# Kernel optimization log

Measured on AMD Instinct MI355X. Metric: run time of the kernel, lower is better.

## Reference

```python
import jax, jax.numpy as jnp
import numpy as np

KS = 5          # B-spline kernel_size per pseudo-coordinate dim
DIM = 2         # pseudo-coordinate dimensionality
NUM_GRAPHS = 64


def spline_conv(x, src, dst, edge_attr, W, root, bias):
    """Degree-1 open B-spline conv (torch-spline-conv semantics, aggr='mean').
    x: [N,Cin], edge_attr: [E,DIM] in [0,1], W: [KS**DIM,Cin,Cout]."""
    N = x.shape[0]
    E = src.shape[0]
    v = edge_attr * (KS - 1)                                   # [E,DIM]
    k_lo = jnp.clip(jnp.floor(v), 0, KS - 2).astype(jnp.int32) # lower knot index
    frac = v - k_lo.astype(v.dtype)                            # [E,DIM]
    # Precompute x @ W_k for all K kernel weights per node: [N,K,Cout]
    xW = jnp.einsum('nc,kco->nko', x, W)
    msg = jnp.zeros((E, W.shape[2]), x.dtype)
    # 2^DIM = 4 nonzero basis products for degree-1 splines
    for bits in ((0, 0), (0, 1), (1, 0), (1, 1)):
        b = jnp.ones((E,), x.dtype)
        wi = jnp.zeros((E,), jnp.int32)
        stride = 1
        for d, bit in enumerate(bits):
            b = b * (frac[:, d] if bit else (1.0 - frac[:, d]))
            wi = wi + (k_lo[:, d] + bit) * stride
            stride *= KS
        msg = msg + b[:, None] * xW[src, wi]                   # gather [E,Cout]
    agg = jax.ops.segment_sum(msg, dst, num_segments=N)
    deg = jax.ops.segment_sum(jnp.ones((E,), x.dtype), dst, num_segments=N)
    agg = agg / jnp.maximum(deg, 1.0)[:, None]                 # mean aggregation
    return agg + x @ root + bias


def setup_inputs() -> dict:
    key = jax.random.key(0)
    ks = jax.random.split(key, 12)
    N, E = 20000, 320000
    Cin, H, O = 1, 32, 10
    K = KS * KS
    p = lambda k, s: jax.random.normal(k, s, jnp.float32) * 0.1
    return {
        'x': jax.random.normal(ks[0], (N, Cin), jnp.float32),
        'edge_attr': jax.random.uniform(ks[1], (E, DIM), jnp.float32),
        'W1': p(ks[2], (K, Cin, H)), 'root1': p(ks[3], (Cin, H)), 'b1': jnp.zeros((H,), jnp.float32),
        'W2': p(ks[4], (K, H, 2 * H)), 'root2': p(ks[5], (H, 2 * H)), 'b2': jnp.zeros((2 * H,), jnp.float32),
        'Wf1': p(ks[6], (2 * H, 128)), 'bf1': jnp.zeros((128,), jnp.float32),
        'Wf2': p(ks[7], (128, O)), 'bf2': jnp.zeros((O,), jnp.float32),
        'edge_index': jax.random.randint(ks[8], (2, E), 0, N),
        'batch': jnp.sort(jax.random.randint(ks[9], (N,), 0, NUM_GRAPHS)),
    }


def reference(x, edge_attr, W1, root1, b1, W2, root2, b2, Wf1, bf1, Wf2, bf2, edge_index, batch):
    src, dst = edge_index[0], edge_index[1]
    h = jax.nn.relu(spline_conv(x, src, dst, edge_attr, W1, root1, b1))
    h = jax.nn.relu(spline_conv(h, src, dst, edge_attr, W2, root2, b2))
    # global mean pool over graphs
    gsum = jax.ops.segment_sum(h, batch, num_segments=NUM_GRAPHS)
    cnt = jax.ops.segment_sum(jnp.ones((h.shape[0],), h.dtype), batch, num_segments=NUM_GRAPHS)
    g = gsum / jnp.maximum(cnt, 1.0)[:, None]
    g = jax.nn.relu(g @ Wf1 + bf1)
    return jax.nn.log_softmax(g @ Wf2 + bf2, axis=1)
```

## Files before the change

kernel.cpp:

```cpp
#include <hip/hip_runtime.h>
#include <hip/hip_fp16.h>
#include <math.h>

#define KK 25
#define H1C 32
#define H2C 64
#define FCC 128
#define NCLS 10
#define NG 64
#define M1 32
#define M2 16
#define NHB 128
#define HBIN 10240

typedef _Float16 v8h __attribute__((ext_vector_type(8)));
typedef float v4f __attribute__((ext_vector_type(4)));

__global__ __launch_bounds__(256) void hist_kernel(
    const int* __restrict__ edge_index, int E, int N,
    int* __restrict__ part) {
    __shared__ int hs[HBIN];
    int b = blockIdx.x, tid = threadIdx.x;
    int per = (E + NHB - 1) / NHB;
    int beg = b * per, end = min(E, beg + per);
    for (int lo = 0; lo < N; lo += HBIN) {
        int sz = min(HBIN, N - lo);
        __syncthreads();
        for (int i = tid; i < sz; i += 256) hs[i] = 0;
        __syncthreads();
        for (int i = beg + tid; i < end; i += 256) {
            int d = edge_index[E + i] - lo;
            if ((unsigned)d < (unsigned)sz) atomicAdd(&hs[d], 1);
        }
        __syncthreads();
        for (int i = tid; i < sz; i += 256) part[(size_t)b * N + lo + i] = hs[i];
    }
}

__global__ void merge_kernel(const int* __restrict__ part, int N,
                             int* __restrict__ degi) {
    int n = blockIdx.x * 256 + threadIdx.x;
    if (n >= N) return;
    int s = 0;
    for (int b = 0; b < NHB; b++) s += part[(size_t)b * N + n];
    degi[n] = s;
}

__global__ void scan1_kernel(const int* __restrict__ degi, int N,
                             int* __restrict__ incl, int* __restrict__ bsum) {
    __shared__ int s[256];
    int tid = threadIdx.x;
    int i = blockIdx.x * 256 + tid;
    int v = (i < N) ? degi[i] : 0;
    s[tid] = v;
    __syncthreads();
    for (int off = 1; off < 256; off <<= 1) {
        int t = (tid >= off) ? s[tid - off] : 0;
        __syncthreads();
        s[tid] += t;
        __syncthreads();
    }
    if (i < N) incl[i] = s[tid];
    if (tid == 255) bsum[blockIdx.x] = s[255];
}

__global__ void scan2_kernel(int* __restrict__ bsum, int nb) {
    __shared__ int s[256];
    int tid = threadIdx.x;
    int v = (tid < nb) ? bsum[tid] : 0;
    s[tid] = v;
    __syncthreads();
    for (int off = 1; off < 256; off <<= 1) {
        int t = (tid >= off) ? s[tid - off] : 0;
        __syncthreads();
        s[tid] += t;
        __syncthreads();
    }
    if (tid < nb) bsum[tid] = s[tid] - v;
}

__global__ void scan3_kernel(const int* __restrict__ incl, const int* __restrict__ degi,
                             const int* __restrict__ bsum, int N,
                             int* __restrict__ rowst, int* __restrict__ cur) {
    int i = blockIdx.x * 256 + threadIdx.x;
    if (i >= N) return;
    int r = incl[i] - degi[i] + bsum[blockIdx.x];
    rowst[i] = r;
    cur[i] = r;
}

__global__ void bucket_kernel(const float* __restrict__ edge_attr,
                              const int* __restrict__ edge_index, int E,
                              int* __restrict__ cur, int4* __restrict__ es) {
    int e = blockIdx.x * blockDim.x + threadIdx.x;
    if (e >= E) return;
    float v0 = edge_attr[2 * e + 0] * 4.0f;
    float v1 = edge_attr[2 * e + 1] * 4.0f;
    int k0 = (int)floorf(v0); k0 = min(max(k0, 0), 3);
    int k1 = (int)floorf(v1); k1 = min(max(k1, 0), 3);
    float f0 = v0 - (float)k0, f1 = v1 - (float)k1;
    int dst = edge_index[E + e];
    int pos = atomicAdd(&cur[dst], 1);
    es[pos] = make_int4(edge_index[e], (dst << 8) | (k0 + 5 * k1),
                        __float_as_int(f0), __float_as_int(f1));
}

__global__ void w2t_kernel(const float* __restrict__ W2, __half* __restrict__ W2t) {
    int idx = blockIdx.x * 256 + threadIdx.x;
    if (idx >= KK * H2C * H1C) return;
    int c = idx & 31, o = (idx >> 5) & 63, k = idx >> 11;
    W2t[idx] = __float2half(W2[(k * H1C + c) * H2C + o]);
}

__global__ __launch_bounds__(256) void l1_kernel(
    const float* __restrict__ x,
    const int* __restrict__ rowst, const int* __restrict__ degi,
    const int4* __restrict__ es,
    const float* __restrict__ W1, const float* __restrict__ root1,
    const float* __restrict__ b1, int N, int E,
    float* __restrict__ h1, __half* __restrict__ h1f) {
    __shared__ float w1s[KK * H1C];
    __shared__ float agg1[M1 * H1C];
    __shared__ int4 eb[8][32];
    __shared__ float xb[8][32];
    int tid = threadIdx.x;
    for (int i = tid; i < KK * H1C; i += 256) w1s[i] = W1[i];
    for (int i = tid; i < M1 * H1C; i += 256) agg1[i] = 0.0f;
    __syncthreads();
    int g = tid >> 5, o = tid & 31;
    int n0 = blockIdx.x * M1;
    int blkBeg = rowst[n0];
    int blkEnd = (n0 + M1 < N) ? rowst[n0 + M1] : E;
    int total = blkEnd - blkBeg;
    int per = (total + 7) >> 3;
    int wBeg = blkBeg + g * per;
    int wEnd = min(blkEnd, wBeg + per);
    int curDst = -1;
    float acc = 0.0f;
    for (int base = wBeg; base < wEnd; base += 32) {
        int m = min(32, wEnd - base);
        if (o < m) {
            int4 ed = es[base + o];
            eb[g][o] = ed;
            xb[g][o] = x[ed.x];
        }
        for (int j = 0; j < m; j++) {
            int4 ed = eb[g][j];
            float xs = xb[g][j];
            int dst = ed.y >> 8;
            if (dst != curDst) {
                if (curDst >= 0) atomicAdd(&agg1[(curDst - n0) * H1C + o], acc);
                acc = 0.0f;
                curDst = dst;
            }
            float f0 = __int_as_float(ed.z), f1 = __int_as_float(ed.w);
            float g0 = 1.0f - f0, g1 = 1.0f - f1;
            int kb = (ed.y & 0xff) << 5;
            float coef = g0 * g1 * w1s[kb + o] + f0 * g1 * w1s[kb + 32 + o] +
                         g0 * f1 * w1s[kb + 160 + o] + f0 * f1 * w1s[kb + 192 + o];
            acc = fmaf(xs, coef, acc);
        }
    }
    if (curDst >= 0) atomicAdd(&agg1[(curDst - n0) * H1C + o], acc);
    __syncthreads();
#pragma unroll
    for (int i = 0; i < 4; i++) {
        int ln = g + 8 * i;
        int n = n0 + ln;
        if (n < N) {
            float rdeg = 1.0f / fmaxf((float)degi[n], 1.0f);
            float hv = fmaxf(agg1[ln * H1C + o] * rdeg + x[n] * root1[o] + b1[o], 0.0f);
            h1[n * H1C + o] = hv;
            h1f[n * H1C + o] = __float2half(hv);
        }
    }
}

__global__ __launch_bounds__(256) void xw2m_kernel(
    const __half* __restrict__ h1f,
    const __half* __restrict__ W2t,
    int N, __half* __restrict__ xph) {
    int wv = threadIdx.x >> 6;
    int lane = threadIdx.x & 63;
    int r15 = lane & 15, quad = lane >> 4;
    int n0 = blockIdx.x * 16;
    int o0 = wv * 16;
    v8h afrag = {};
    int an = n0 + r15;
    if (an < N) afrag = *(const v8h*)(h1f + (size_t)an * H1C + quad * 8);
    for (int k = 0; k < KK; k++) {
        v8h bfrag = *(const v8h*)(W2t + ((k << 6) + o0 + r15) * H1C + quad * 8);
        v4f acc = {};
        acc = __builtin_amdgcn_mfma_f32_16x16x32_f16(afrag, bfrag, acc, 0, 0, 0);
#pragma unroll
        for (int r = 0; r < 4; r++) {
            int mn = n0 + quad * 4 + r;
            if (mn < N)
                xph[(size_t)mn * (KK * H2C) + (k << 6) + o0 + r15] = __float2half(acc[r]);
        }
    }
}

__global__ __launch_bounds__(256) void l2_kernel(
    const float* __restrict__ h1,
    const int* __restrict__ rowst, const int* __restrict__ degi,
    const int4* __restrict__ es,
    const unsigned* __restrict__ xphu,
    const float* __restrict__ root2, const float* __restrict__ b2,
    const int* __restrict__ batch,
    int N, int E, float* __restrict__ gsum) {
    __shared__ float agg[M2 * H2C];
    __shared__ int4 eb[4][64];
    int tid = threadIdx.x;
    for (int i = tid; i < M2 * H2C; i += 256) agg[i] = 0.0f;
    __syncthreads();
    int w = tid >> 6, lane = tid & 63;
    int o2 = lane & 31, eh = lane >> 5;
    int n0 = blockIdx.x * M2;
    int blkBeg = rowst[n0];
    int blkEnd = (n0 + M2 < N) ? rowst[n0 + M2] : E;
    int total = blkEnd - blkBeg;
    int per = (total + 3) >> 2;
    int wBeg = blkBeg + w * per;
    int wEnd = min(blkEnd, wBeg + per);
    int curDst = -1;
    float ax = 0.0f, ay = 0.0f;
    for (int base = wBeg; base < wEnd; base += 64) {
        int m = min(64, wEnd - base);
        if (lane < m) eb[w][lane] = es[base + lane];
        for (int j = 0; j < m; j += 2) {
            int jj = j + eh;
            bool act = jj < m;
            int4 ed = eb[w][act ? jj : j];
            const unsigned* p = xphu + (size_t)ed.x * (KK * H2C / 2) +
                                ((ed.y & 0xff) << 5) + o2;
            unsigned t0 = p[0], t1 = p[32], t2 = p[160], t3 = p[192];
            if (act) {
                int dst = ed.y >> 8;
                if (dst != curDst) {
                    if (curDst >= 0) {
                        atomicAdd(&agg[(curDst - n0) * H2C + 2 * o2], ax);
                        atomicAdd(&agg[(curDst - n0) * H2C + 2 * o2 + 1], ay);
                    }
                    ax = ay = 0.0f;
                    curDst = dst;
                }
                float f0 = __int_as_float(ed.z), f1 = __int_as_float(ed.w);
                float g0 = 1.0f - f0, g1 = 1.0f - f1;
                float b0 = g0 * g1, b1 = f0 * g1, bb2 = g0 * f1, b3 = f0 * f1;
                __half2 h0 = *(__half2*)&t0, h1v = *(__half2*)&t1;
                __half2 h2 = *(__half2*)&t2, h3 = *(__half2*)&t3;
                ax = fmaf(b0, __low2float(h0), ax);  ay = fmaf(b0, __high2float(h0), ay);
                ax = fmaf(b1, __low2float(h1v), ax); ay = fmaf(b1, __high2float(h1v), ay);
                ax = fmaf(bb2, __low2float(h2), ax); ay = fmaf(bb2, __high2float(h2), ay);
                ax = fmaf(b3, __low2float(h3), ax);  ay = fmaf(b3, __high2float(h3), ay);
            }
        }
    }
    if (curDst >= 0) {
        atomicAdd(&agg[(curDst - n0) * H2C + 2 * o2], ax);
        atomicAdd(&agg[(curDst - n0) * H2C + 2 * o2 + 1], ay);
    }
    __syncthreads();

#pragma unroll
    for (int i = 0; i < 4; i++) {
        int ln = w + 4 * i;
        int n = n0 + ln;
        if (n < N) {
            float rd = 1.0f / fmaxf((float)degi[n], 1.0f);
            float v = agg[ln * H2C + lane] * rd + b2[lane];
            const float* hr = h1 + n * H1C;
#pragma unroll 8
            for (int c = 0; c < H1C; c++) v = fmaf(hr[c], root2[c * H2C + lane], v);
            agg[ln * H2C + lane] = fmaxf(v, 0.0f);
        } else {
            agg[ln * H2C + lane] = 0.0f;
        }
    }
    __syncthreads();

    if (tid < H2C) {
        float run = 0.0f;
        int curg = batch[n0];
        for (int ln = 0; ln < M2; ln++) {
            int n = n0 + ln;
            if (n >= N) break;
            int gg = batch[n];
            if (gg != curg) {
                atomicAdd(&gsum[curg * H2C + tid], run);
                run = 0.0f;
                curg = gg;
            }
            run += agg[ln * H2C + tid];
        }
        atomicAdd(&gsum[curg * H2C + tid], run);
    }
}

__global__ void head_kernel(const float* __restrict__ gsum,
                            const int* __restrict__ batch, int N,
                            const float* __restrict__ Wf1, const float* __restrict__ bf1,
                            const float* __restrict__ Wf2, const float* __restrict__ bf2,
                            float* __restrict__ out) {
    __shared__ float gc[H2C];
    __shared__ float t1[FCC];
    __shared__ float lg[NCLS];
    __shared__ float lse;
    __shared__ float scnt;
    int g = blockIdx.x, tid = threadIdx.x;
    if (tid == 0) {
        int lo = 0, hi = N;
        while (lo < hi) { int m = (lo + hi) >> 1; if (batch[m] < g) lo = m + 1; else hi = m; }
        int lb = lo;
        lo = 0; hi = N;
        while (lo < hi) { int m = (lo + hi) >> 1; if (batch[m] <= g) lo = m + 1; else hi = m; }
        scnt = (float)(lo - lb);
    }
    __syncthreads();
    if (tid < H2C) gc[tid] = gsum[g * H2C + tid] / fmaxf(scnt, 1.0f);
    __syncthreads();
    {
        float acc = bf1[tid];
        for (int c = 0; c < H2C; c++) acc += gc[c] * Wf1[c * FCC + tid];
        t1[tid] = fmaxf(acc, 0.0f);
    }
    __syncthreads();
    if (tid < NCLS) {
        float acc = bf2[tid];
        for (int j = 0; j < FCC; j++) acc += t1[j] * Wf2[j * NCLS + tid];
        lg[tid] = acc;
    }
    __syncthreads();
    if (tid == 0) {
        float m = lg[0];
        for (int c = 1; c < NCLS; c++) m = fmaxf(m, lg[c]);
        float s = 0.0f;
        for (int c = 0; c < NCLS; c++) s += expf(lg[c] - m);
        lse = m + logf(s);
    }
    __syncthreads();
    if (tid < NCLS) out[g * NCLS + tid] = lg[tid] - lse;
}

extern "C" void kernel_launch(void* const* d_in, const int* in_sizes, int n_in,
                              void* d_out, int out_size, void* d_ws, size_t ws_size,
                              hipStream_t stream) {
    const float* x          = (const float*)d_in[0];
    const float* edge_attr  = (const float*)d_in[1];
    const float* W1         = (const float*)d_in[2];
    const float* root1      = (const float*)d_in[3];
    const float* b1         = (const float*)d_in[4];
    const float* W2         = (const float*)d_in[5];
    const float* root2      = (const float*)d_in[6];
    const float* b2         = (const float*)d_in[7];
    const float* Wf1        = (const float*)d_in[8];
    const float* bf1        = (const float*)d_in[9];
    const float* Wf2        = (const float*)d_in[10];
    const float* bf2        = (const float*)d_in[11];
    const int*   edge_index = (const int*)d_in[12];
    const int*   batch      = (const int*)d_in[13];
    float* out = (float*)d_out;

    const int N = in_sizes[13];
    const int E = in_sizes[12] / 2;
    const int NB = (N + 255) / 256;

    int4*     es   = (int4*)d_ws;
    unsigned* xphu = (unsigned*)(es + E);
    __half*   w2t  = (__half*)(xphu + (size_t)N * 800);
    __half*   h1f  = w2t + KK * H2C * H1C;
    float* gsum  = (float*)(h1f + (size_t)N * H1C);
    int*   degi  = (int*)(gsum + NG * H2C);
    int*   rowst = degi + N;
    int*   cur   = rowst + N;
    int*   incl  = cur + N;
    int*   bsum  = incl + N;
    float* h1    = (float*)(bsum + 256);
    int*   part  = (int*)(h1 + (size_t)N * H1C);

    hipMemsetAsync(gsum, 0, (size_t)NG * H2C * sizeof(float), stream);

    hist_kernel<<<NHB, 256, 0, stream>>>(edge_index, E, N, part);
    merge_kernel<<<NB, 256, 0, stream>>>(part, N, degi);

    scan1_kernel<<<NB, 256, 0, stream>>>(degi, N, incl, bsum);
    scan2_kernel<<<1, 256, 0, stream>>>(bsum, NB);
    scan3_kernel<<<NB, 256, 0, stream>>>(incl, degi, bsum, N, rowst, cur);

    bucket_kernel<<<(E + 255) / 256, 256, 0, stream>>>(edge_attr, edge_index, E, cur, es);
    w2t_kernel<<<(KK * H2C * H1C + 255) / 256, 256, 0, stream>>>(W2, w2t);

    l1_kernel<<<(N + M1 - 1) / M1, 256, 0, stream>>>(
        x, rowst, degi, es, W1, root1, b1, N, E, h1, h1f);

    xw2m_kernel<<<(N + 15) / 16, 256, 0, stream>>>(h1f, w2t, N, (__half*)xphu);

    l2_kernel<<<(N + M2 - 1) / M2, 256, 0, stream>>>(
        h1, rowst, degi, es, xphu, root2, b2, batch, N, E, gsum);

    head_kernel<<<NG, FCC, 0, stream>>>(gsum, batch, N, Wf1, bf1, Wf2, bf2, out);
}
```

Baseline: 211.9 us.

## Replace histogram degree count with global atomics and fuse W2 transpose

```diff
diff --git a/kernel.cpp b/kernel.cpp
--- a/kernel.cpp
+++ b/kernel.cpp
@@ -10,40 +10,21 @@
 #define NG 64
 #define M1 32
 #define M2 16
-#define NHB 128
-#define HBIN 10240
 
 typedef _Float16 v8h __attribute__((ext_vector_type(8)));
+typedef _Float16 v4h __attribute__((ext_vector_type(4)));
 typedef float v4f __attribute__((ext_vector_type(4)));
 
-__global__ __launch_bounds__(256) void hist_kernel(
-    const int* __restrict__ edge_index, int E, int N,
-    int* __restrict__ part) {
-    __shared__ int hs[HBIN];
-    int b = blockIdx.x, tid = threadIdx.x;
-    int per = (E + NHB - 1) / NHB;
-    int beg = b * per, end = min(E, beg + per);
-    for (int lo = 0; lo < N; lo += HBIN) {
-        int sz = min(HBIN, N - lo);
-        __syncthreads();
-        for (int i = tid; i < sz; i += 256) hs[i] = 0;
-        __syncthreads();
-        for (int i = beg + tid; i < end; i += 256) {
-            int d = edge_index[E + i] - lo;
-            if ((unsigned)d < (unsigned)sz) atomicAdd(&hs[d], 1);
-        }
-        __syncthreads();
-        for (int i = tid; i < sz; i += 256) part[(size_t)b * N + lo + i] = hs[i];
-    }
-}
-
-__global__ void merge_kernel(const int* __restrict__ part, int N,
-                             int* __restrict__ degi) {
-    int n = blockIdx.x * 256 + threadIdx.x;
-    if (n >= N) return;
-    int s = 0;
-    for (int b = 0; b < NHB; b++) s += part[(size_t)b * N + n];
-    degi[n] = s;
+__global__ __launch_bounds__(256) void deg_kernel(
+    const int* __restrict__ edge_index, int E,
+    int* __restrict__ degi,
+    const float* __restrict__ W2, __half* __restrict__ W2t) {
+    int i = blockIdx.x * 256 + threadIdx.x;
+    if (i < KK * H2C * H1C) {
+        int c = i & 31, o = (i >> 5) & 63, k = i >> 11;
+        W2t[i] = __float2half(W2[(k * H1C + c) * H2C + o]);
+    }
+    if (i < E) atomicAdd(&degi[edge_index[E + i]], 1);
 }
 
 __global__ void scan1_kernel(const int* __restrict__ degi, int N,
@@ -103,13 +84,6 @@
     int pos = atomicAdd(&cur[dst], 1);
     es[pos] = make_int4(edge_index[e], (dst << 8) | (k0 + 5 * k1),
                         __float_as_int(f0), __float_as_int(f1));
-}
-
-__global__ void w2t_kernel(const float* __restrict__ W2, __half* __restrict__ W2t) {
-    int idx = blockIdx.x * 256 + threadIdx.x;
-    if (idx >= KK * H2C * H1C) return;
-    int c = idx & 31, o = (idx >> 5) & 63, k = idx >> 11;
-    W2t[idx] = __float2half(W2[(k * H1C + c) * H2C + o]);
 }
 
 __global__ __launch_bounds__(256) void l1_kernel(
@@ -185,18 +159,22 @@
     int r15 = lane & 15, quad = lane >> 4;
     int n0 = blockIdx.x * 16;
     int o0 = wv * 16;
-    v8h afrag = {};
-    int an = n0 + r15;
-    if (an < N) afrag = *(const v8h*)(h1f + (size_t)an * H1C + quad * 8);
+    v8h bfrag = {};
+    int bn = n0 + r15;
+    bool wr = bn < N;
+    if (wr) bfrag = *(const v8h*)(h1f + (size_t)bn * H1C + quad * 8);
+    size_t baseoff = (size_t)bn * (KK * H2C) + o0 + (quad << 2);
     for (int k = 0; k < KK; k++) {
-        v8h bfrag = *(const v8h*)(W2t + ((k << 6) + o0 + r15) * H1C + quad * 8);
+        v8h afrag = *(const v8h*)(W2t + ((k << 6) + o0 + r15) * H1C + quad * 8);
         v4f acc = {};
         acc = __builtin_amdgcn_mfma_f32_16x16x32_f16(afrag, bfrag, acc, 0, 0, 0);
-#pragma unroll
-        for (int r = 0; r < 4; r++) {
-            int mn = n0 + quad * 4 + r;
-            if (mn < N)
-                xph[(size_t)mn * (KK * H2C) + (k << 6) + o0 + r15] = __float2half(acc[r]);
+        if (wr) {
+            v4h hv;
+            hv[0] = (_Float16)acc[0];
+            hv[1] = (_Float16)acc[1];
+            hv[2] = (_Float16)acc[2];
+            hv[3] = (_Float16)acc[3];
+            *(v4h*)(xph + baseoff + (k << 6)) = hv;
         }
     }
 }
@@ -377,19 +355,19 @@
     int*   incl  = cur + N;
     int*   bsum  = incl + N;
     float* h1    = (float*)(bsum + 256);
-    int*   part  = (int*)(h1 + (size_t)N * H1C);
-
-    hipMemsetAsync(gsum, 0, (size_t)NG * H2C * sizeof(float), stream);
-
-    hist_kernel<<<NHB, 256, 0, stream>>>(edge_index, E, N, part);
-    merge_kernel<<<NB, 256, 0, stream>>>(part, N, degi);
+
+    hipMemsetAsync(gsum, 0, (size_t)NG * H2C * sizeof(float) + (size_t)N * sizeof(int),
+                   stream);
+
+    const int W2TN = KK * H2C * H1C;
+    int degBlocks = (max(E, W2TN) + 255) / 256;
+    deg_kernel<<<degBlocks, 256, 0, stream>>>(edge_index, E, degi, W2, w2t);
 
     scan1_kernel<<<NB, 256, 0, stream>>>(degi, N, incl, bsum);
     scan2_kernel<<<1, 256, 0, stream>>>(bsum, NB);
     scan3_kernel<<<NB, 256, 0, stream>>>(incl, degi, bsum, N, rowst, cur);
 
     bucket_kernel<<<(E + 255) / 256, 256, 0, stream>>>(edge_attr, edge_index, E, cur, es);
-    w2t_kernel<<<(KK * H2C * H1C + 255) / 256, 256, 0, stream>>>(W2, w2t);
 
     l1_kernel<<<(N + M1 - 1) / M1, 256, 0, stream>>>(
         x, rowst, degi, es, W1, root1, b1, N, E, h1, h1f);
```

Result: no change. 215.4 us (+1.7%).
